# Kernel optimization log

Measured on AMD Instinct MI355X. Metric: run time of the kernel, lower is better.

## Reference

```python
import jax, jax.numpy as jnp
import numpy as np
from jax import lax

EPS = 1e-5

def _bsign(w):
    # Binarize to {-1,+1} with straight-through estimator (identity grad), as in BNN training.
    b = jnp.where(w >= 0, 1.0, -1.0).astype(w.dtype)
    return w + lax.stop_gradient(b - w)

def _hardtanh(x):
    return jnp.clip(x, -1.0, 1.0)

def _maxpool2(x):
    return lax.reduce_window(x, -jnp.inf, lax.max, (1, 1, 2, 2), (1, 1, 2, 2), 'VALID')

def _bn(x, g, b, axes):
    m = jnp.mean(x, axis=axes, keepdims=True)
    v = jnp.mean(jnp.square(x - m), axis=axes, keepdims=True)
    xn = (x - m) * lax.rsqrt(v + EPS)
    if x.ndim == 4:
        return xn * g[None, :, None, None] + b[None, :, None, None]
    return xn * g[None, :] + b[None, :]

def _conv_block(x, w, bias, g, bt, pool):
    # ReplicationPad2d(1) -> binarized 3x3 conv -> (maxpool) -> BatchNorm2d
    x = jnp.pad(x, ((0, 0), (0, 0), (1, 1), (1, 1)), mode='edge')
    x = lax.conv_general_dilated(x, _bsign(w), (1, 1), 'VALID',
                                 dimension_numbers=('NCHW', 'OIHW', 'NCHW'))
    x = x + bias[None, :, None, None]
    if pool:
        x = _maxpool2(x)
    return _bn(x, g, bt, (0, 2, 3))

def setup_inputs() -> dict:
    key = jax.random.key(0)
    cnt = [0]
    def nk():
        cnt[0] += 1
        return jax.random.fold_in(key, cnt[0])
    def rn(shape, s=0.05):
        return (jax.random.normal(nk(), shape, dtype=jnp.float32) * s)
    d = {'x': jax.random.normal(nk(), (256, 3, 32, 32), dtype=jnp.float32)}
    chans = [(3, 128), (128, 128), (128, 256), (256, 256), (256, 512), (512, 512)]
    for i, (ci, co) in enumerate(chans, 1):
        d[f'cw{i}'] = rn((co, ci, 3, 3))
        d[f'cb{i}'] = jnp.zeros((co,), jnp.float32)
        d[f'g{i}'] = jnp.ones((co,), jnp.float32)
        d[f'bt{i}'] = jnp.zeros((co,), jnp.float32)
    fdims = [(512 * 16, 1536), (1536, 1536), (1536, 10)]
    for i, (fi, fo) in enumerate(fdims, 1):
        d[f'w{i}'] = rn((fo, fi))
        d[f'b{i}'] = jnp.zeros((fo,), jnp.float32)
        d[f'gl{i}'] = jnp.ones((fo,), jnp.float32)
        d[f'bl{i}'] = jnp.zeros((fo,), jnp.float32)
    return d

def reference(x, cw1, cb1, g1, bt1, cw2, cb2, g2, bt2, cw3, cb3, g3, bt3,
              cw4, cb4, g4, bt4, cw5, cb5, g5, bt5, cw6, cb6, g6, bt6,
              w1, b1, gl1, bl1, w2, b2, gl2, bl2, w3, b3, gl3, bl3):
    x = _hardtanh(_conv_block(x, cw1, cb1, g1, bt1, False))
    x = _hardtanh(_conv_block(x, cw2, cb2, g2, bt2, True))
    x = _hardtanh(_conv_block(x, cw3, cb3, g3, bt3, False))
    x = _hardtanh(_conv_block(x, cw4, cb4, g4, bt4, True))
    x = _hardtanh(_conv_block(x, cw5, cb5, g5, bt5, False))
    x = _hardtanh(_conv_block(x, cw6, cb6, g6, bt6, True))
    x = x.reshape(x.shape[0], 512 * 4 * 4)
    x = _hardtanh(_bn(x @ _bsign(w1).T + b1, gl1, bl1, (0,)))
    x = _hardtanh(_bn(x @ _bsign(w2).T + b2, gl2, bl2, (0,)))
    x = _bn(x @ _bsign(w3).T + b3, gl3, bl3, (0,))
    return x
```

## Files before the change

### kernel.cpp

```cpp
#include <hip/hip_runtime.h>
#include <stdint.h>

typedef unsigned short u16;
typedef unsigned int   u32;
typedef __attribute__((ext_vector_type(8))) short bf16x8;
typedef __attribute__((ext_vector_type(4))) float f32x4;

__device__ __forceinline__ float b2f(u16 u){ u32 i = ((u32)u) << 16; float f; __builtin_memcpy(&f,&i,4); return f; }
__device__ __forceinline__ u16 f2b(float f){ u32 i; __builtin_memcpy(&i,&f,4); i += 0x7FFFu + ((i>>16)&1u); return (u16)(i>>16); }

__global__ void k_prep_wfrag_conv(const float* __restrict__ w, u16* __restrict__ wf,
                                  int Cout, int Cin, int KT){
  int NCT = Cout >> 4;
  int total = KT*NCT*512;
  int Kmax = 9*Cin;
  for(int i = blockIdx.x*256 + threadIdx.x; i < total; i += gridDim.x*256){
    int i8 = i & 7; int lane = (i>>3)&63; int t = i>>9;
    int ct = t % NCT; int kt = t / NCT;
    int k = kt*32 + ((lane>>4)<<3) + i8;
    int co = (ct<<4) + (lane&15);
    u16 v = 0;
    if(k < Kmax){
      int tap = k / Cin; int ci = k - tap*Cin;
      v = (w[(size_t)(co*Cin+ci)*9 + tap] >= 0.f) ? (u16)0x3F80 : (u16)0xBF80;
    }
    wf[i] = v;
  }
}
__global__ void k_prep_wfrag_fc(const float* __restrict__ w, u16* __restrict__ wf,
                                int Nf, int K, int NCTp, int permute){
  int total = (K>>5)*NCTp*512;
  for(int i = blockIdx.x*256 + threadIdx.x; i < total; i += gridDim.x*256){
    int i8 = i & 7; int lane = (i>>3)&63; int t = i>>9;
    int ct = t % NCTp; int kt = t / NCTp;
    int k = kt*32 + ((lane>>4)<<3) + i8;
    int n = (ct<<4) + (lane&15);
    u16 v = 0;
    if(n < Nf){
      int kr = permute ? ((k & 511)*16 + (k >> 9)) : k;
      v = (w[(size_t)n*K + kr] >= 0.f) ? (u16)0x3F80 : (u16)0xBF80;
    }
    wf[i] = v;
  }
}

__global__ void k_pad_input(const float* __restrict__ x, u16* __restrict__ p){
  int total = 256*34*34*3;
  for(int i = blockIdx.x*256 + threadIdx.x; i < total; i += gridDim.x*256){
    int c = i % 3; int t = i / 3; int wp = t % 34; t /= 34; int hp = t % 34; int n = t / 34;
    int h = hp-1; h = h<0?0:(h>31?31:h);
    int w = wp-1; w = w<0?0:(w>31?31:w);
    p[i] = f2b(x[((size_t)(n*3+c)*32 + h)*32 + w]);
  }
}

__global__ void k_im2col(const u16* __restrict__ xp, u16* __restrict__ AI){
  int m = blockIdx.x*256 + threadIdx.x;
  int w = m & 31; int h = (m>>5)&31; int n = m>>10;
  u16 buf[32];
  #pragma unroll
  for(int j=27;j<32;j++) buf[j]=0;
  #pragma unroll
  for(int tap=0;tap<9;tap++){
    int dh=tap/3, dw=tap-dh*3;
    const u16* s = xp + ((size_t)(n*34 + h+dh)*34 + (w+dw))*3;
    buf[tap*3+0]=s[0]; buf[tap*3+1]=s[1]; buf[tap*3+2]=s[2];
  }
  uint4* d = (uint4*)(AI + (size_t)m*32);
  const uint4* b4 = (const uint4*)buf;
  d[0]=b4[0]; d[1]=b4[1]; d[2]=b4[2]; d[3]=b4[3];
}

template<int MF,int NF,int CS,int W,int POOL,int STATS>
__global__ __launch_bounds__(256) void k_conv_t(
    const u16* __restrict__ xp, const u16* __restrict__ wf, const float* __restrict__ bias,
    float* __restrict__ y, float* __restrict__ SP,
    int Cin, int NCT, int coutOff, int yOff, int yC)
{
  extern __shared__ u16 lds[];
  __shared__ float sbuf[STATS ? 4*NF*16 : 4];
  constexpr int BM = 2*MF*16;
  constexpr int R  = BM / W;
  constexpr int Wp = W + 2;
  constexpr int S  = CS + 8;
  constexpr int c32cnt = CS >> 5;
  constexpr int c32log = (CS==256)?3:((CS==128)?2:1);
  constexpr int csLog  = (CS==256)?8:((CS==128)?7:6);
  constexpr int wLog   = (W==32)?5:((W==16)?4:3);
  constexpr int hblocks = W / R;
  constexpr int NKt = 9*c32cnt;
  constexpr int BN = 2*NF*16;

  const int tid = threadIdx.x, lane = tid&63, wid = tid>>6;
  const int wm = wid&1, wn = wid>>1;
  const int n  = blockIdx.x / hblocks;
  const int h0 = (blockIdx.x % hblocks) * R;
  const int cb = coutOff + blockIdx.y*BN;
  const int KTall = Cin >> 5;
  const int halves = Cin / CS;
  const int ctb = (cb>>4) + wn*NF;

  int offA[MF];
  #pragma unroll
  for(int fm=0; fm<MF; fm++){
    int p = (wm*MF+fm)*16 + (lane & 15);
    int rl = p >> wLog; int w_ = p & (W-1);
    offA[fm] = (rl*Wp + w_)*S + ((lane>>4)<<3);
  }

  f32x4 acc[MF][NF];
  #pragma unroll
  for(int i=0;i<MF;i++)
    #pragma unroll
    for(int j=0;j<NF;j++) acc[i][j] = (f32x4){0.f,0.f,0.f,0.f};

  constexpr int total8 = ((R+2)*Wp*CS) >> 3;

  for(int hv=0; hv<halves; hv++){
    __syncthreads();
    {
      const u16* gx = xp + ((size_t)(n*(W+2) + h0))*(size_t)(Wp*Cin) + (size_t)hv*CS;
      for(int i8=tid; i8<total8; i8+=256){
        int e = i8 << 3; int pix = e >> csLog; int ci = e & (CS-1);
        *(uint4*)(lds + pix*S + ci) = *(const uint4*)(gx + (size_t)pix*Cin + ci);
      }
    }
    __syncthreads();
    const int ktb = (hv*CS) >> 5;

    auto loadf = [&](int i, bf16x8 (&AF)[MF], bf16x8 (&BF)[NF]){
      int tap = i >> c32log; int c32 = i & (c32cnt-1);
      int dh = (tap*11) >> 5; int dw = tap - dh*3;
      int kt = tap*KTall + ktb + c32;
      const u16* bp = wf + (((size_t)kt*NCT + ctb)*64 + lane)*8;
      #pragma unroll
      for(int fn=0;fn<NF;fn++) BF[fn] = *(const bf16x8*)(bp + fn*512);
      const int toff = (dh*Wp + dw)*S + (c32<<5);
      #pragma unroll
      for(int fm=0;fm<MF;fm++) AF[fm] = *(const bf16x8*)(lds + offA[fm] + toff);
    };
    auto domf = [&](bf16x8 (&AF)[MF], bf16x8 (&BF)[NF]){
      #pragma unroll
      for(int fm=0;fm<MF;fm++)
        #pragma unroll
        for(int fn=0;fn<NF;fn++)
          acc[fm][fn] = __builtin_amdgcn_mfma_f32_16x16x32_bf16(AF[fm],BF[fn],acc[fm][fn],0,0,0);
    };

    bf16x8 Aa[MF], Ba[NF], Ab[MF], Bb2[NF];
    loadf(0, Aa, Ba);
    for(int i=0; i<NKt; i+=2){
      loadf(i+1, Ab, Bb2);
      domf(Aa, Ba);
      int nx = i+2; if(nx > NKt-1) nx = NKt-1;
      loadf(nx, Aa, Ba);
      domf(Ab, Bb2);
    }
  }

  const int col = lane & 15, g = lane >> 4, rowq = g << 2;
  float sarr[NF], qarr[NF];
  #pragma unroll
  for(int fn=0; fn<NF; fn++){
    const int coutG = cb + (wn*NF+fn)*16 + col;
    const float bs = bias[coutG];
    const int cl = coutG - yOff;
    float vals[MF][4];
    #pragma unroll
    for(int fm=0;fm<MF;fm++)
      #pragma unroll
      for(int ri=0;ri<4;ri++) vals[fm][ri] = acc[fm][fn][ri] + bs;

    float s = 0.f, q = 0.f;
    if constexpr (!POOL){
      #pragma unroll
      for(int fm=0;fm<MF;fm++){
        #pragma unroll
        for(int ri=0;ri<4;ri++){
          int p = (wm*MF+fm)*16 + rowq + ri;
          int rl = p >> wLog; int w_ = p & (W-1);
          y[(((size_t)n*W + h0+rl)*W + w_)*(size_t)yC + cl] = vals[fm][ri];
          if constexpr (STATS){ s += vals[fm][ri]; q += vals[fm][ri]*vals[fm][ri]; }
        }
      }
    } else {
      constexpr int HO = W/2;
      if constexpr (W==32){
        #pragma unroll
        for(int pp=0;pp<2;pp++){
          float pv[4];
          #pragma unroll
          for(int ri=0;ri<4;ri++) pv[ri] = fmaxf(vals[pp][ri], vals[pp+2][ri]);
          float po0 = fmaxf(pv[0],pv[1]), po1 = fmaxf(pv[2],pv[3]);
          int pr = (h0>>1) + wm;
          int wo = pp*8 + (rowq>>1);
          size_t base = (((size_t)n*HO + pr)*HO + wo)*(size_t)yC + cl;
          y[base] = po0; y[base + yC] = po1;
          if constexpr (STATS){ s += po0 + po1; q += po0*po0 + po1*po1; }
        }
      } else if constexpr (W==16){
        #pragma unroll
        for(int pp=0;pp<2;pp++){
          float pv[4];
          #pragma unroll
          for(int ri=0;ri<4;ri++) pv[ri] = fmaxf(vals[2*pp][ri], vals[2*pp+1][ri]);
          float po0 = fmaxf(pv[0],pv[1]), po1 = fmaxf(pv[2],pv[3]);
          int pr = (h0>>1) + wm*2 + pp;
          int wo = (rowq>>1);
          size_t base = (((size_t)n*HO + pr)*HO + wo)*(size_t)yC + cl;
          y[base] = po0; y[base + yC] = po1;
          if constexpr (STATS){ s += po0 + po1; q += po0*po0 + po1*po1; }
        }
      } else {
        #pragma unroll
        for(int fm=0;fm<2;fm++){
          float pv[4];
          #pragma unroll
          for(int ri=0;ri<4;ri++){
            float o = __shfl_xor(vals[fm][ri], 32);
            pv[ri] = fmaxf(vals[fm][ri], o);
          }
          if(g < 2){
            float po0 = fmaxf(pv[0],pv[1]), po1 = fmaxf(pv[2],pv[3]);
            int pr = wm*2 + fm;
            int wo = g*2;
            size_t base = (((size_t)n*HO + pr)*HO + wo)*(size_t)yC + cl;
            y[base] = po0; y[base + yC] = po1;
            if constexpr (STATS){ s += po0 + po1; q += po0*po0 + po1*po1; }
          }
        }
      }
    }
    if constexpr (STATS){
      s += __shfl_xor(s, 16); s += __shfl_xor(s, 32);
      q += __shfl_xor(q, 16); q += __shfl_xor(q, 32);
      sarr[fn] = s; qarr[fn] = q;
    }
  }
  if constexpr (STATS){
    if(wm==1 && lane<16){
      #pragma unroll
      for(int fn=0;fn<NF;fn++){
        int lc = (wn*NF+fn)*16 + col;
        sbuf[lc] = sarr[fn]; sbuf[BN+lc] = qarr[fn];
      }
    }
    __syncthreads();
    if(wm==0 && lane<16){
      #pragma unroll
      for(int fn=0;fn<NF;fn++){
        int lc = (wn*NF+fn)*16 + col;
        int cl = cb + (wn*NF+fn)*16 + col - yOff;
        SP[(size_t)blockIdx.x*2*yC + cl]      = sarr[fn] + sbuf[lc];
        SP[(size_t)blockIdx.x*2*yC + yC + cl] = qarr[fn] + sbuf[BN+lc];
      }
    }
  }
}

__global__ __launch_bounds__(256) void k_gemm_c1(
    const u16* __restrict__ A, const u16* __restrict__ wf, const float* __restrict__ bias,
    float* __restrict__ y, float* __restrict__ SP, int K, int NCT, int yC, int coutOff, int yOff)
{
  __shared__ float sb[128];
  const int tid = threadIdx.x; const int lane = tid & 63; const int wid = tid >> 6;
  const int wm = wid & 1, wn = wid >> 1;
  const int mb = blockIdx.x*64;
  const int col = lane & 15;
  f32x4 acc[2][2];
  #pragma unroll
  for(int i=0;i<2;i++){ acc[i][0]=(f32x4){0.f,0.f,0.f,0.f}; acc[i][1]=(f32x4){0.f,0.f,0.f,0.f}; }
  const u16* a0p = A + (size_t)(mb + wm*32 + col)*K + ((lane>>4)<<3);
  const u16* a1p = a0p + (size_t)16*K;
  const int ct = (coutOff>>4) + wn*2;
  const int KT = K >> 5;
  for(int kt=0; kt<KT; kt++){
    bf16x8 a0 = *(const bf16x8*)(a0p + (size_t)kt*32);
    bf16x8 a1 = *(const bf16x8*)(a1p + (size_t)kt*32);
    const u16* bp = wf + (((size_t)kt*NCT + ct)*64 + lane)*8;
    bf16x8 b0 = *(const bf16x8*)(bp);
    bf16x8 b1 = *(const bf16x8*)(bp + 512);
    acc[0][0] = __builtin_amdgcn_mfma_f32_16x16x32_bf16(a0,b0,acc[0][0],0,0,0);
    acc[0][1] = __builtin_amdgcn_mfma_f32_16x16x32_bf16(a0,b1,acc[0][1],0,0,0);
    acc[1][0] = __builtin_amdgcn_mfma_f32_16x16x32_bf16(a1,b0,acc[1][0],0,0,0);
    acc[1][1] = __builtin_amdgcn_mfma_f32_16x16x32_bf16(a1,b1,acc[1][1],0,0,0);
  }
  const int rowq = (lane>>4)<<2;
  float sarr[2], qarr[2];
  #pragma unroll
  for(int fn=0; fn<2; fn++){
    int coutG = wn*32 + fn*16 + col + coutOff;
    float bs = bias[coutG];
    int cl = coutG - yOff;
    float s=0.f, q=0.f;
    #pragma unroll
    for(int fm=0; fm<2; fm++){
      #pragma unroll
      for(int ri=0; ri<4; ri++){
        int m = mb + wm*32 + fm*16 + rowq + ri;
        float v = acc[fm][fn][ri] + bs;
        y[(size_t)m*yC + cl] = v;
        s += v; q += v*v;
      }
    }
    s += __shfl_xor(s, 16); s += __shfl_xor(s, 32);
    q += __shfl_xor(q, 16); q += __shfl_xor(q, 32);
    sarr[fn]=s; qarr[fn]=q;
  }
  if(wm==1 && lane<16){
    #pragma unroll
    for(int fn=0;fn<2;fn++){ int lc = wn*32+fn*16+col; sb[lc]=sarr[fn]; sb[64+lc]=qarr[fn]; }
  }
  __syncthreads();
  if(wm==0 && lane<16){
    #pragma unroll
    for(int fn=0;fn<2;fn++){
      int lc = wn*32+fn*16+col;
      SP[(size_t)blockIdx.x*2*yC + lc]      = sarr[fn] + sb[lc];
      SP[(size_t)blockIdx.x*2*yC + yC + lc] = qarr[fn] + sb[64+lc];
    }
  }
}

__global__ __launch_bounds__(256) void k_gemm_part(
    const u16* __restrict__ A, const u16* __restrict__ wf, float* __restrict__ P,
    int M, int K, int NCT, int ncp, int KTC)
{
  const int tid = threadIdx.x; const int lane = tid & 63; const int wid = tid >> 6;
  const int wm = wid & 1, wn = wid >> 1;
  const int mb = blockIdx.x*64, nb = blockIdx.y*64, kz = blockIdx.z;
  const int col = lane & 15;
  f32x4 acc[2][2];
  #pragma unroll
  for(int i=0;i<2;i++){ acc[i][0]=(f32x4){0.f,0.f,0.f,0.f}; acc[i][1]=(f32x4){0.f,0.f,0.f,0.f}; }
  const u16* a0p = A + (size_t)(mb + wm*32 + col)*K + ((lane>>4)<<3);
  const u16* a1p = a0p + (size_t)16*K;
  const int kt0 = kz*KTC;
  for(int t=0; t<KTC; t++){
    int kt = kt0 + t;
    bf16x8 a0 = *(const bf16x8*)(a0p + (size_t)kt*32);
    bf16x8 a1 = *(const bf16x8*)(a1p + (size_t)kt*32);
    const u16* bp = wf + (((size_t)kt*NCT + (nb>>4) + wn*2)*64 + lane)*8;
    bf16x8 b0 = *(const bf16x8*)(bp);
    bf16x8 b1 = *(const bf16x8*)(bp + 512);
    acc[0][0] = __builtin_amdgcn_mfma_f32_16x16x32_bf16(a0,b0,acc[0][0],0,0,0);
    acc[0][1] = __builtin_amdgcn_mfma_f32_16x16x32_bf16(a0,b1,acc[0][1],0,0,0);
    acc[1][0] = __builtin_amdgcn_mfma_f32_16x16x32_bf16(a1,b0,acc[1][0],0,0,0);
    acc[1][1] = __builtin_amdgcn_mfma_f32_16x16x32_bf16(a1,b1,acc[1][1],0,0,0);
  }
  const int rowq = (lane>>4)<<2;
  #pragma unroll
  for(int fm=0; fm<2; fm++){
    #pragma unroll
    for(int fn=0; fn<2; fn++){
      int mbase = mb + wm*32 + fm*16 + rowq;
      int c = nb + wn*32 + fn*16 + col;
      *(f32x4*)(P + ((size_t)kz*ncp + c)*M + mbase) = acc[fm][fn];
    }
  }
}

__global__ __launch_bounds__(256) void k_fc_fuse(
    const float* __restrict__ P, const float* __restrict__ bias,
    const float* __restrict__ g, const float* __restrict__ bt,
    u16* __restrict__ outb, float* __restrict__ outf,
    int Nf, int ncp, int CH, int clampF)
{
  __shared__ float sb[10];
  const int nf = blockIdx.x; const int m = threadIdx.x;
  float v = bias[nf];
  for(int z=0; z<CH; z++) v += P[((size_t)z*ncp + nf)*256 + m];
  float s = v, q = v*v;
  #pragma unroll
  for(int d=1; d<64; d<<=1){ s += __shfl_xor(s,d); q += __shfl_xor(q,d); }
  if((m&63)==0){ sb[m>>6]=s; sb[4+(m>>6)]=q; }
  __syncthreads();
  if(m==0){
    float st=sb[0]+sb[1]+sb[2]+sb[3], qt=sb[4]+sb[5]+sb[6]+sb[7];
    float mean=st*(1.f/256.f); float var=qt*(1.f/256.f)-mean*mean;
    float A=g[nf]*rsqrtf(var+1e-5f);
    sb[8]=A; sb[9]=bt[nf]-mean*A;
  }
  __syncthreads();
  float o = v*sb[8]+sb[9];
  if(clampF) o = fminf(fmaxf(o,-1.f),1.f);
  if(outb) outb[(size_t)m*Nf+nf] = f2b(o);
  else     outf[(size_t)m*Nf+nf] = o;
}

__global__ void k_bn_prep2(const float* __restrict__ part, const float* __restrict__ g,
                           const float* __restrict__ bt, float* __restrict__ AB,
                           int C, int rows, float invCnt, int cbase, int Cfull){
  __shared__ float ls[512];
  int c = blockIdx.x; int tid = threadIdx.x;
  float s=0.f, q=0.f;
  for(int r=tid; r<rows; r+=256){ s += part[(size_t)r*2*C + c]; q += part[(size_t)r*2*C + C + c]; }
  ls[tid]=s; ls[256+tid]=q; __syncthreads();
  for(int st=128; st>0; st>>=1){
    if(tid<st){ ls[tid]+=ls[tid+st]; ls[256+tid]+=ls[256+tid+st]; }
    __syncthreads();
  }
  if(tid==0){
    float m = ls[0]*invCnt; float v = ls[256]*invCnt - m*m;
    float A = g[c]*rsqrtf(v + 1e-5f);
    AB[cbase+c] = A; AB[Cfull+cbase+c] = bt[c] - m*A;
  }
}

__global__ void k_bn_act_f32(const float* __restrict__ in, const float* __restrict__ Aa,
                             const float* __restrict__ Bb, u16* __restrict__ out,
                             int Cbuf, int rows, int HO, int WO, int Cfull, int cbase,
                             int padMode, int clampF){
  int cpg = Cbuf >> 3;
  int total = rows * cpg;
  for(int i = blockIdx.x*256 + threadIdx.x; i < total; i += gridDim.x*256){
    int c8 = i % cpg; int row = i / cpg; int c0 = c8*8;
    float4 v0 = *(const float4*)(in + (size_t)i*8);
    float4 v1 = *(const float4*)(in + (size_t)i*8 + 4);
    float4 A0 = *(const float4*)(Aa + c0);
    float4 A1 = *(const float4*)(Aa + c0 + 4);
    float4 B0 = *(const float4*)(Bb + c0);
    float4 B1 = *(const float4*)(Bb + c0 + 4);
    float f[8];
    f[0]=v0.x*A0.x+B0.x; f[1]=v0.y*A0.y+B0.y; f[2]=v0.z*A0.z+B0.z; f[3]=v0.w*A0.w+B0.w;
    f[4]=v1.x*A1.x+B1.x; f[5]=v1.y*A1.y+B1.y; f[6]=v1.z*A1.z+B1.z; f[7]=v1.w*A1.w+B1.w;
    if(clampF){
      #pragma unroll
      for(int j=0;j<8;j++) f[j] = fminf(fmaxf(f[j], -1.f), 1.f);
    }
    uint4 o;
    o.x = (u32)f2b(f[0]) | ((u32)f2b(f[1])<<16);
    o.y = (u32)f2b(f[2]) | ((u32)f2b(f[3])<<16);
    o.z = (u32)f2b(f[4]) | ((u32)f2b(f[5])<<16);
    o.w = (u32)f2b(f[6]) | ((u32)f2b(f[7])<<16);
    if(!padMode){
      *(uint4*)(out + (size_t)row*Cbuf + c0) = o;
    } else {
      int w = row % WO; int t = row / WO; int h = t % HO; int n = t / HO;
      int Wp2 = WO + 2;
      size_t base = (size_t)n*(HO+2)*Wp2;
      #define WRP(hp,wp) *(uint4*)(out + ((base + (size_t)(hp)*Wp2 + (wp))*(size_t)Cfull) + cbase + c0) = o
      WRP(h+1, w+1);
      if(h==0)            WRP(0,    w+1);
      if(h==HO-1)         WRP(HO+1, w+1);
      if(w==0)            WRP(h+1,  0);
      if(w==WO-1)         WRP(h+1,  WO+1);
      if(h==0    && w==0)    WRP(0,    0);
      if(h==0    && w==WO-1) WRP(0,    WO+1);
      if(h==HO-1 && w==0)    WRP(HO+1, 0);
      if(h==HO-1 && w==WO-1) WRP(HO+1, WO+1);
      #undef WRP
    }
  }
}

extern "C" void kernel_launch(void* const* d_in, const int* in_sizes, int n_in,
                              void* d_out, int out_size, void* d_ws, size_t ws_size,
                              hipStream_t stream) {
  (void)in_sizes; (void)n_in; (void)out_size; (void)ws_size;
  const float* x = (const float*)d_in[0];
  const float *cw[6], *cb[6], *cgam[6], *cbt[6];
  for(int i=0;i<6;i++){
    cw[i]  =(const float*)d_in[1+4*i];
    cb[i]  =(const float*)d_in[2+4*i];
    cgam[i]=(const float*)d_in[3+4*i];
    cbt[i] =(const float*)d_in[4+4*i];
  }
  const float *fw[3], *fbias[3], *fg[3], *fbt[3];
  for(int i=0;i<3;i++){
    fw[i]   =(const float*)d_in[25+4*i];
    fbias[i]=(const float*)d_in[26+4*i];
    fg[i]   =(const float*)d_in[27+4*i];
    fbt[i]  =(const float*)d_in[28+4*i];
  }

  char* ws = (char*)d_ws;
  size_t off = 0;
  auto alloc = [&](size_t bytes){ size_t o = off; off = (off + bytes + 255) & ~(size_t)255; return o; };
  const size_t oX  = alloc((size_t)256*34*34*3*2);
  const size_t oP  = alloc((size_t)256*34*34*128*2);
  const size_t oP2 = alloc((size_t)256*18*18*128*2);
  const size_t oYf = alloc((size_t)67108864);
  const size_t oQf = alloc((size_t)16777216);
  const int CinA[6]  = {3,128,128,256,256,512};
  const int CoutA[6] = {128,128,256,256,512,512};
  const int KTA[6]   = {1,36,36,72,72,144};
  size_t oWc[6];
  for(int l=0;l<6;l++) oWc[l] = alloc((size_t)KTA[l]*(CoutA[l]>>4)*512*2);
  const size_t oSP = alloc((size_t)4096*128*4);
  const size_t oAB = alloc((size_t)2*1536*4);

  u16*   X    = (u16*)(ws + oX);
  u16*   Pb   = (u16*)(ws + oP);
  u16*   P2   = (u16*)(ws + oP2);
  float* Yf   = (float*)(ws + oYf);
  u16*   AI   = (u16*)(ws + oQf);
  u16*   F0   = (u16*)(ws + oQf);
  float* SP   = (float*)(ws + oSP);
  float* AB   = (float*)(ws + oAB);
  float* Pg   = (float*)(ws + oYf + (size_t)32*1024*1024);
  u16*   FAa  = (u16*)(ws + oYf + (size_t)58*1024*1024);
  u16*   FBa  = (u16*)(ws + oYf + (size_t)60*1024*1024);
  u16* Wf1 = (u16*)(ws + oP);
  u16* Wf2 = (u16*)(ws + oP + (size_t)26*1024*1024);
  u16* Wf3 = (u16*)(ws + oP + (size_t)31*1024*1024);

  for(int l=0;l<6;l++)
    k_prep_wfrag_conv<<<1024,256,0,stream>>>(cw[l], (u16*)(ws+oWc[l]), CoutA[l], CinA[l], KTA[l]);
  k_pad_input<<<2048,256,0,stream>>>(x, X);
  k_im2col<<<1024,256,0,stream>>>(X, AI);

  for(int h=0; h<2; h++){
    k_gemm_c1<<<4096,256,0,stream>>>(AI, (u16*)(ws+oWc[0]), cb[0], Yf, SP, 32, 8, 64, h*64, h*64);
    k_bn_prep2<<<64,256,0,stream>>>(SP, cgam[0]+h*64, cbt[0]+h*64, AB, 64, 4096, 1.0f/262144.0f, h*64, 128);
    k_bn_act_f32<<<2048,256,0,stream>>>(Yf, AB+h*64, AB+128+h*64, Pb, 64, 262144, 32, 32, 128, h*64, 1, 1);
  }
  k_conv_t<4,2,64,32,1,1><<<dim3(2048,2),256,29376,stream>>>(Pb, (u16*)(ws+oWc[1]), cb[1], Yf, SP, 128, 8, 0, 0, 128);
  k_bn_prep2<<<128,256,0,stream>>>(SP, cgam[1], cbt[1], AB, 128, 2048, 1.0f/65536.0f, 0, 128);
  k_bn_act_f32<<<2048,256,0,stream>>>(Yf, AB, AB+128, P2, 128, 65536, 16, 16, 128, 0, 1, 1);
  k_conv_t<4,4,128,16,0,1><<<dim3(512,2),256,48960,stream>>>(P2, (u16*)(ws+oWc[2]), cb[2], Yf, SP, 128, 16, 0, 0, 256);
  k_bn_prep2<<<256,256,0,stream>>>(SP, cgam[2], cbt[2], AB, 256, 512, 1.0f/65536.0f, 0, 256);
  k_bn_act_f32<<<2048,256,0,stream>>>(Yf, AB, AB+256, Pb, 256, 65536, 16, 16, 256, 0, 1, 1);
  k_conv_t<4,4,128,16,1,1><<<dim3(512,2),256,48960,stream>>>(Pb, (u16*)(ws+oWc[3]), cb[3], Yf, SP, 256, 16, 0, 0, 256);
  k_bn_prep2<<<256,256,0,stream>>>(SP, cgam[3], cbt[3], AB, 256, 512, 1.0f/16384.0f, 0, 256);
  k_bn_act_f32<<<2048,256,0,stream>>>(Yf, AB, AB+256, P2, 256, 16384, 8, 8, 256, 0, 1, 1);
  k_conv_t<2,4,128,8,0,1><<<dim3(256,4),256,27200,stream>>>(P2, (u16*)(ws+oWc[4]), cb[4], Yf, SP, 256, 32, 0, 0, 512);
  k_bn_prep2<<<512,256,0,stream>>>(SP, cgam[4], cbt[4], AB, 512, 256, 1.0f/16384.0f, 0, 512);
  k_bn_act_f32<<<2048,256,0,stream>>>(Yf, AB, AB+512, Pb, 512, 16384, 8, 8, 512, 0, 1, 1);
  k_conv_t<2,4,128,8,1,1><<<dim3(256,4),256,27200,stream>>>(Pb, (u16*)(ws+oWc[5]), cb[5], Yf, SP, 512, 32, 0, 0, 512);
  k_bn_prep2<<<512,256,0,stream>>>(SP, cgam[5], cbt[5], AB, 512, 256, 1.0f/4096.0f, 0, 512);
  k_bn_act_f32<<<512,256,0,stream>>>(Yf, AB, AB+512, F0, 512, 4096, 4, 4, 512, 0, 0, 1);

  k_prep_wfrag_fc<<<2048,256,0,stream>>>(fw[0], Wf1, 1536, 8192, 96, 1);
  k_prep_wfrag_fc<<<1024,256,0,stream>>>(fw[1], Wf2, 1536, 1536, 96, 0);
  k_prep_wfrag_fc<<<64,256,0,stream>>>  (fw[2], Wf3, 10,   1536, 4,  0);

  k_gemm_part<<<dim3(4,24,16),256,0,stream>>>(F0, Wf1, Pg, 256, 8192, 96, 1536, 16);
  k_fc_fuse<<<1536,256,0,stream>>>(Pg, fbias[0], fg[0], fbt[0], FAa, nullptr, 1536, 1536, 16, 1);
  k_gemm_part<<<dim3(4,24,8),256,0,stream>>>(FAa, Wf2, Pg, 256, 1536, 96, 1536, 6);
  k_fc_fuse<<<1536,256,0,stream>>>(Pg, fbias[1], fg[1], fbt[1], FBa, nullptr, 1536, 1536, 8, 1);
  k_gemm_part<<<dim3(4,1,4),256,0,stream>>>(FBa, Wf3, Pg, 256, 1536, 4, 64, 12);
  k_fc_fuse<<<10,256,0,stream>>>(Pg, fbias[2], fg[2], fbt[2], nullptr, (float*)d_out, 10, 64, 4, 0);
}
```

Measured before the change: 853.2 us.

## Fuse conv1 BN/act into recomputed GEMM and shrink conv tiles for more blocks

Layer 1 now runs its tiny K=32 GEMM twice. The first pass only accumulates per-channel statistics. The second recomputes the GEMM and applies bias, BN, hardtanh, bf16 conversion and edge-replicated padding directly into the padded activation buffer. This removes the fp32 intermediate write and reread and the separate bn_act kernel, at the cost of a redundant GEMM. Separately, conv layers 3-6 use smaller N tiles (64 instead of 128) with more grid blocks and less shared memory, aiming for better occupancy and CU fill.

```diff
diff --git a/kernel.cpp b/kernel.cpp
--- a/kernel.cpp
+++ b/kernel.cpp
@@ -258,14 +258,17 @@
   }
 }
 
+template<int MODE>
 __global__ __launch_bounds__(256) void k_gemm_c1(
     const u16* __restrict__ A, const u16* __restrict__ wf, const float* __restrict__ bias,
-    float* __restrict__ y, float* __restrict__ SP, int K, int NCT, int yC, int coutOff, int yOff)
+    float* __restrict__ SP, const float* __restrict__ AB, u16* __restrict__ outp,
+    int K, int NCT, int yC)
 {
   __shared__ float sb[128];
   const int tid = threadIdx.x; const int lane = tid & 63; const int wid = tid >> 6;
   const int wm = wid & 1, wn = wid >> 1;
   const int mb = blockIdx.x*64;
+  const int coutOff = blockIdx.y*64;
   const int col = lane & 15;
   f32x4 acc[2][2];
   #pragma unroll
@@ -286,38 +289,68 @@
     acc[1][1] = __builtin_amdgcn_mfma_f32_16x16x32_bf16(a1,b1,acc[1][1],0,0,0);
   }
   const int rowq = (lane>>4)<<2;
-  float sarr[2], qarr[2];
-  #pragma unroll
-  for(int fn=0; fn<2; fn++){
-    int coutG = wn*32 + fn*16 + col + coutOff;
-    float bs = bias[coutG];
-    int cl = coutG - yOff;
-    float s=0.f, q=0.f;
+  if constexpr (MODE == 0){
+    float sarr[2], qarr[2];
     #pragma unroll
-    for(int fm=0; fm<2; fm++){
-      #pragma unroll
-      for(int ri=0; ri<4; ri++){
-        int m = mb + wm*32 + fm*16 + rowq + ri;
-        float v = acc[fm][fn][ri] + bs;
-        y[(size_t)m*yC + cl] = v;
-        s += v; q += v*v;
-      }
-    }
-    s += __shfl_xor(s, 16); s += __shfl_xor(s, 32);
-    q += __shfl_xor(q, 16); q += __shfl_xor(q, 32);
-    sarr[fn]=s; qarr[fn]=q;
-  }
-  if(wm==1 && lane<16){
+    for(int fn=0; fn<2; fn++){
+      int coutG = wn*32 + fn*16 + col + coutOff;
+      float bs = bias[coutG];
+      float s=0.f, q=0.f;
+      #pragma unroll
+      for(int fm=0; fm<2; fm++){
+        #pragma unroll
+        for(int ri=0; ri<4; ri++){
+          float v = acc[fm][fn][ri] + bs;
+          s += v; q += v*v;
+        }
+      }
+      s += __shfl_xor(s, 16); s += __shfl_xor(s, 32);
+      q += __shfl_xor(q, 16); q += __shfl_xor(q, 32);
+      sarr[fn]=s; qarr[fn]=q;
+    }
+    if(wm==1 && lane<16){
+      #pragma unroll
+      for(int fn=0;fn<2;fn++){ int lc = wn*32+fn*16+col; sb[lc]=sarr[fn]; sb[64+lc]=qarr[fn]; }
+    }
+    __syncthreads();
+    if(wm==0 && lane<16){
+      #pragma unroll
+      for(int fn=0;fn<2;fn++){
+        int lc = wn*32+fn*16+col;
+        int cl = coutOff + lc;
+        SP[(size_t)blockIdx.x*2*yC + cl]      = sarr[fn] + sb[lc];
+        SP[(size_t)blockIdx.x*2*yC + yC + cl] = qarr[fn] + sb[64+lc];
+      }
+    }
+  } else {
     #pragma unroll
-    for(int fn=0;fn<2;fn++){ int lc = wn*32+fn*16+col; sb[lc]=sarr[fn]; sb[64+lc]=qarr[fn]; }
-  }
-  __syncthreads();
-  if(wm==0 && lane<16){
-    #pragma unroll
-    for(int fn=0;fn<2;fn++){
-      int lc = wn*32+fn*16+col;
-      SP[(size_t)blockIdx.x*2*yC + lc]      = sarr[fn] + sb[lc];
-      SP[(size_t)blockIdx.x*2*yC + yC + lc] = qarr[fn] + sb[64+lc];
+    for(int fn=0; fn<2; fn++){
+      int c = wn*32 + fn*16 + col + coutOff;
+      float bs = bias[c];
+      float Ac = AB[c], Bc = AB[128 + c];
+      #pragma unroll
+      for(int fm=0; fm<2; fm++){
+        #pragma unroll
+        for(int ri=0; ri<4; ri++){
+          int m = mb + wm*32 + fm*16 + rowq + ri;
+          int w = m & 31, h = (m>>5)&31, n = m>>10;
+          float o = (acc[fm][fn][ri] + bs)*Ac + Bc;
+          o = fminf(fmaxf(o, -1.f), 1.f);
+          u16 b = f2b(o);
+          u16* ob = outp + (size_t)n*34*34*128;
+          #define WR1(hp,wp) ob[((size_t)(hp)*34 + (wp))*128 + c] = b
+          WR1(h+1, w+1);
+          if(h==0)        WR1(0,  w+1);
+          if(h==31)       WR1(33, w+1);
+          if(w==0)        WR1(h+1, 0);
+          if(w==31)       WR1(h+1, 33);
+          if(h==0 && w==0)   WR1(0, 0);
+          if(h==0 && w==31)  WR1(0, 33);
+          if(h==31 && w==0)  WR1(33, 0);
+          if(h==31 && w==31) WR1(33, 33);
+          #undef WR1
+        }
+      }
     }
   }
 }
@@ -487,7 +520,7 @@
   const int KTA[6]   = {1,36,36,72,72,144};
   size_t oWc[6];
   for(int l=0;l<6;l++) oWc[l] = alloc((size_t)KTA[l]*(CoutA[l]>>4)*512*2);
-  const size_t oSP = alloc((size_t)4096*128*4);
+  const size_t oSP = alloc((size_t)4096*256*4);
   const size_t oAB = alloc((size_t)2*1536*4);
 
   u16*   X    = (u16*)(ws + oX);
@@ -510,24 +543,23 @@
   k_pad_input<<<2048,256,0,stream>>>(x, X);
   k_im2col<<<1024,256,0,stream>>>(X, AI);
 
-  for(int h=0; h<2; h++){
-    k_gemm_c1<<<4096,256,0,stream>>>(AI, (u16*)(ws+oWc[0]), cb[0], Yf, SP, 32, 8, 64, h*64, h*64);
-    k_bn_prep2<<<64,256,0,stream>>>(SP, cgam[0]+h*64, cbt[0]+h*64, AB, 64, 4096, 1.0f/262144.0f, h*64, 128);
-    k_bn_act_f32<<<2048,256,0,stream>>>(Yf, AB+h*64, AB+128+h*64, Pb, 64, 262144, 32, 32, 128, h*64, 1, 1);
-  }
+  k_gemm_c1<0><<<dim3(4096,2),256,0,stream>>>(AI, (u16*)(ws+oWc[0]), cb[0], SP, nullptr, nullptr, 32, 8, 128);
+  k_bn_prep2<<<128,256,0,stream>>>(SP, cgam[0], cbt[0], AB, 128, 4096, 1.0f/262144.0f, 0, 128);
+  k_gemm_c1<1><<<dim3(4096,2),256,0,stream>>>(AI, (u16*)(ws+oWc[0]), cb[0], nullptr, AB, Pb, 32, 8, 128);
+
   k_conv_t<4,2,64,32,1,1><<<dim3(2048,2),256,29376,stream>>>(Pb, (u16*)(ws+oWc[1]), cb[1], Yf, SP, 128, 8, 0, 0, 128);
   k_bn_prep2<<<128,256,0,stream>>>(SP, cgam[1], cbt[1], AB, 128, 2048, 1.0f/65536.0f, 0, 128);
   k_bn_act_f32<<<2048,256,0,stream>>>(Yf, AB, AB+128, P2, 128, 65536, 16, 16, 128, 0, 1, 1);
-  k_conv_t<4,4,128,16,0,1><<<dim3(512,2),256,48960,stream>>>(P2, (u16*)(ws+oWc[2]), cb[2], Yf, SP, 128, 16, 0, 0, 256);
+  k_conv_t<4,2,64,16,0,1><<<dim3(512,4),256,25920,stream>>>(P2, (u16*)(ws+oWc[2]), cb[2], Yf, SP, 128, 16, 0, 0, 256);
   k_bn_prep2<<<256,256,0,stream>>>(SP, cgam[2], cbt[2], AB, 256, 512, 1.0f/65536.0f, 0, 256);
   k_bn_act_f32<<<2048,256,0,stream>>>(Yf, AB, AB+256, Pb, 256, 65536, 16, 16, 256, 0, 1, 1);
-  k_conv_t<4,4,128,16,1,1><<<dim3(512,2),256,48960,stream>>>(Pb, (u16*)(ws+oWc[3]), cb[3], Yf, SP, 256, 16, 0, 0, 256);
+  k_conv_t<4,2,64,16,1,1><<<dim3(512,4),256,25920,stream>>>(Pb, (u16*)(ws+oWc[3]), cb[3], Yf, SP, 256, 16, 0, 0, 256);
   k_bn_prep2<<<256,256,0,stream>>>(SP, cgam[3], cbt[3], AB, 256, 512, 1.0f/16384.0f, 0, 256);
   k_bn_act_f32<<<2048,256,0,stream>>>(Yf, AB, AB+256, P2, 256, 16384, 8, 8, 256, 0, 1, 1);
-  k_conv_t<2,4,128,8,0,1><<<dim3(256,4),256,27200,stream>>>(P2, (u16*)(ws+oWc[4]), cb[4], Yf, SP, 256, 32, 0, 0, 512);
+  k_conv_t<2,2,64,8,0,1><<<dim3(256,8),256,14400,stream>>>(P2, (u16*)(ws+oWc[4]), cb[4], Yf, SP, 256, 32, 0, 0, 512);
   k_bn_prep2<<<512,256,0,stream>>>(SP, cgam[4], cbt[4], AB, 512, 256, 1.0f/16384.0f, 0, 512);
   k_bn_act_f32<<<2048,256,0,stream>>>(Yf, AB, AB+512, Pb, 512, 16384, 8, 8, 512, 0, 1, 1);
-  k_conv_t<2,4,128,8,1,1><<<dim3(256,4),256,27200,stream>>>(Pb, (u16*)(ws+oWc[5]), cb[5], Yf, SP, 512, 32, 0, 0, 512);
+  k_conv_t<2,2,64,8,1,1><<<dim3(256,8),256,14400,stream>>>(Pb, (u16*)(ws+oWc[5]), cb[5], Yf, SP, 512, 32, 0, 0, 512);
   k_bn_prep2<<<512,256,0,stream>>>(SP, cgam[5], cbt[5], AB, 512, 256, 1.0f/4096.0f, 0, 512);
   k_bn_act_f32<<<512,256,0,stream>>>(Yf, AB, AB+512, F0, 512, 4096, 4, 4, 512, 0, 0, 1);
 
```

Result: faster. 823.3 us (-3.5%).
